# Optimization experiments

Hardware: AMD Instinct MI355X
Metric: run time of the kernel (lower is better)

Reference implementation:

```python
import jax, jax.numpy as jnp
import numpy as np

N, M, E = 50000, 50000, 1600000
D_IN, HID, OUT = 128, 128, 128


def setup_inputs() -> dict:
    key = jax.random.key(0)
    ks = jax.random.split(key, 8)
    query = jax.random.normal(ks[0], (N, D_IN), jnp.float32)
    memory = jax.random.normal(ks[1], (M, D_IN), jnp.float32)
    adj_vals = jnp.ones((E,), jnp.float32)  # tf.sparse adjacency values (typically 1.0)
    Wq = jax.random.normal(ks[2], (D_IN, HID), jnp.float32) * 0.05
    bq = jnp.zeros((HID,), jnp.float32)
    Wk = jax.random.normal(ks[3], (D_IN, HID), jnp.float32) * 0.05
    bk = jnp.zeros((HID,), jnp.float32)
    Wv = jax.random.normal(ks[4], (D_IN, OUT), jnp.float32) * 0.05
    bv = jnp.zeros((OUT,), jnp.float32)
    rows = jnp.sort(jax.random.randint(ks[5], (E,), 0, N, jnp.int32))
    cols = jax.random.randint(ks[6], (E,), 0, M, jnp.int32)
    return {"query": query, "memory": memory, "adj_vals": adj_vals,
            "Wq": Wq, "bq": bq, "Wk": Wk, "bk": bk, "Wv": Wv, "bv": bv,
            "rows": rows, "cols": cols}


def reference(query, memory, adj_vals, Wq, bq, Wk, bk, Wv, bv, rows, cols):
    n = query.shape[0]
    hid = Wq.shape[1]
    # Dense projections with gelu (tfa.activations.gelu default approximate=True)
    q = jax.nn.gelu(query @ Wq + bq, approximate=True)   # [n, hid]
    k = jax.nn.gelu(memory @ Wk + bk, approximate=True)  # [m, hid]
    v = jax.nn.gelu(memory @ Wv + bv, approximate=True)  # [m, out]
    # Edge-level scores = (q_i . k_j) / sqrt(hid) * adj_val  (== coef * adj_matrix)
    scores = jnp.sum(q[rows] * k[cols], axis=-1)          # [E]
    scores = scores * (adj_vals / jnp.sqrt(jnp.float32(hid)))
    # Sparse softmax over nonzero entries of each row (tf.sparse.softmax)
    row_max = jax.ops.segment_max(scores, rows, num_segments=n, indices_are_sorted=True)
    row_max = jnp.where(jnp.isfinite(row_max), row_max, 0.0)  # rows with no edges
    e = jnp.exp(scores - row_max[rows])
    denom = jax.ops.segment_sum(e, rows, num_segments=n, indices_are_sorted=True)
    w = e / denom[rows]                                   # [E]
    # Sparse-dense matmul: out_i = sum_j w_ij * v_j
    out = jax.ops.segment_sum(w[:, None] * v[cols], rows, num_segments=n, indices_are_sorted=True)
    return out
```

## Files before the change

### kernel.cpp

```cpp
#include <hip/hip_runtime.h>
#include <math.h>

typedef _Float16 f16x4 __attribute__((ext_vector_type(4)));
typedef _Float16 f16x8 __attribute__((ext_vector_type(8)));
typedef float f32x4 __attribute__((ext_vector_type(4)));

#define DIM 128
#define LDST 136

#if defined(__has_builtin)
#if __has_builtin(__builtin_amdgcn_sdot4)
#define HAVE_SDOT4 1
#endif
#endif

__device__ __forceinline__ int dot4i8(int a, int b, int c) {
#ifdef HAVE_SDOT4
    return __builtin_amdgcn_sdot4(a, b, c, false);
#else
    int s = c;
#pragma unroll
    for (int j = 0; j < 4; ++j)
        s += (int)((signed char)((a >> (8 * j)) & 0xff)) *
             (int)((signed char)((b >> (8 * j)) & 0xff));
    return s;
#endif
}

__device__ __forceinline__ float i8f(unsigned int w, int j) {
    return (float)((signed char)((w >> (8 * j)) & 0xff));
}

__global__ __launch_bounds__(256) void setup_kernel(
    const float* __restrict__ Wq, const float* __restrict__ Wk,
    const float* __restrict__ Wv, _Float16* __restrict__ Wt,
    const int* __restrict__ rows, int* __restrict__ row_ptr, int n, int e)
{
    int b = blockIdx.x;
    if (b < 192) {
        int mat = b >> 6;
        const float* W = (mat == 0) ? Wq : (mat == 1) ? Wk : Wv;
        _Float16* dst = Wt + (size_t)mat * DIM * DIM;
        int idx = (b & 63) * 256 + threadIdx.x;
        int k = idx >> 7;
        int c = idx & 127;
        dst[c * DIM + k] = (_Float16)W[idx];
    } else {
        int r = (b - 192) * 256 + threadIdx.x;
        if (r > n) return;
        if (r == n) { row_ptr[n] = e; return; }
        int lo = 0, hi = e;
        while (lo < hi) {
            int mid = (lo + hi) >> 1;
            if (rows[mid] < r) lo = mid + 1; else hi = mid;
        }
        row_ptr[r] = lo;
    }
}

__global__ __launch_bounds__(256, 3) void proj_gemm_kernel(
    const float* __restrict__ query, const float* __restrict__ memory,
    const _Float16* __restrict__ Wt,
    const float* __restrict__ bq, const float* __restrict__ bk,
    const float* __restrict__ bv,
    unsigned char* __restrict__ q8i, float* __restrict__ sclq,
    unsigned char* __restrict__ k8i, unsigned char* __restrict__ v8i,
    float2* __restrict__ scl2, int n, int m)
{
    __shared__ _Float16 xs[128 * LDST];

    int which = blockIdx.y;
    const float* X     = (which == 0) ? query : memory;
    const _Float16* Wm = Wt + (size_t)which * DIM * DIM;
    const float* bias  = (which == 0) ? bq : (which == 1) ? bk : bv;
    int R              = (which == 0) ? n : m;

    int tid = threadIdx.x;
    int rowblock = blockIdx.x * 128;
    if (rowblock >= R) return;

    for (int it = 0; it < 16; ++it) {
        int flat = it * 256 + tid;
        int r  = flat >> 5;
        int c4 = (flat & 31) * 4;
        int gr = rowblock + r;
        if (gr >= R) gr = R - 1;
        float4 x = *(const float4*)(X + (size_t)gr * DIM + c4);
        f16x4 w4;
        w4[0] = (_Float16)x.x; w4[1] = (_Float16)x.y;
        w4[2] = (_Float16)x.z; w4[3] = (_Float16)x.w;
        *(f16x4*)(&xs[r * LDST + c4]) = w4;
    }
    __syncthreads();

    int wave = tid >> 6;
    int lane = tid & 63;
    int quad = lane >> 4;
    int l16  = lane & 15;
    int wrow = wave * 32;

    f16x8 afrag[2][4];
    for (int rt = 0; rt < 2; ++rt)
        for (int ks = 0; ks < 4; ++ks)
            afrag[rt][ks] = *(const f16x8*)(&xs[(wrow + rt * 16 + l16) * LDST + quad * 8 + ks * 32]);

    f32x4 acc[8][2];
    for (int ct = 0; ct < 8; ++ct) { acc[ct][0] = {0,0,0,0}; acc[ct][1] = {0,0,0,0}; }
    for (int ct = 0; ct < 8; ++ct) {
        const _Float16* wp = Wm + (size_t)(ct * 16 + l16) * DIM + quad * 8;
        for (int ks = 0; ks < 4; ++ks) {
            f16x8 b = *(const f16x8*)(wp + ks * 32);
            acc[ct][0] = __builtin_amdgcn_mfma_f32_16x16x32_f16(afrag[0][ks], b, acc[ct][0], 0, 0, 0);
            acc[ct][1] = __builtin_amdgcn_mfma_f32_16x16x32_f16(afrag[1][ks], b, acc[ct][1], 0, 0, 0);
        }
    }

    __syncthreads();
    for (int ct = 0; ct < 8; ++ct) {
        float bval = bias[ct * 16 + l16];
        for (int rt = 0; rt < 2; ++rt) {
            for (int reg = 0; reg < 4; ++reg) {
                float x = acc[ct][rt][reg] + bval;
                float t  = 0.7978845608028654f * (x + 0.044715f * x * x * x);
                float th = 1.0f - 2.0f / (__expf(2.0f * t) + 1.0f);
                float g  = 0.5f * x * (1.0f + th);
                xs[(wrow + rt * 16 + quad * 4 + reg) * LDST + ct * 16 + l16] = (_Float16)g;
            }
        }
    }
    __syncthreads();

    unsigned char* Y = (which == 0) ? q8i : (which == 1) ? k8i : v8i;
    for (int it = 0; it < 8; ++it) {
        int flat = it * 256 + tid;
        int r  = flat >> 4;
        int c8 = (flat & 15) * 8;
        int gr = rowblock + r;
        f16x8 h = *(const f16x8*)(&xs[r * LDST + c8]);
        float f[8];
        float mx = 0.0f;
#pragma unroll
        for (int j = 0; j < 8; ++j) {
            f[j] = (float)h[j];
            mx = fmaxf(mx, fabsf(f[j]));
        }
        mx = fmaxf(mx, __shfl_xor(mx, 1));
        mx = fmaxf(mx, __shfl_xor(mx, 2));
        mx = fmaxf(mx, __shfl_xor(mx, 4));
        mx = fmaxf(mx, __shfl_xor(mx, 8));
        float qs = (mx > 0.0f) ? 127.0f / mx : 0.0f;
        if (gr < R) {
            unsigned int w0 = 0, w1 = 0;
#pragma unroll
            for (int j = 0; j < 4; ++j) {
                int q = (int)rintf(fminf(fmaxf(f[j] * qs, -127.0f), 127.0f));
                w0 |= ((unsigned int)(q & 0xff)) << (8 * j);
            }
#pragma unroll
            for (int j = 0; j < 4; ++j) {
                int q = (int)rintf(fminf(fmaxf(f[4 + j] * qs, -127.0f), 127.0f));
                w1 |= ((unsigned int)(q & 0xff)) << (8 * j);
            }
            *(uint2*)(Y + (size_t)gr * DIM + c8) = make_uint2(w0, w1);
            if ((flat & 15) == 0) {
                float ds = mx * (1.0f / 127.0f);
                if (which == 0)      sclq[gr]   = ds;
                else if (which == 1) scl2[gr].x = ds;
                else                 scl2[gr].y = ds;
            }
        }
    }
}

__global__ __launch_bounds__(256) void edge_attn_kernel(
    const unsigned char* __restrict__ q8i, const float* __restrict__ sclq,
    const unsigned char* __restrict__ k8i, const unsigned char* __restrict__ v8i,
    const float2* __restrict__ scl2, const float* __restrict__ adj_vals,
    const int* __restrict__ cols, const int* __restrict__ row_ptr,
    float* __restrict__ out, int n)
{
    int row = blockIdx.x * 4 + (threadIdx.x >> 6);
    if (row >= n) return;
    int lane = threadIdx.x & 63;
    int g    = lane >> 3;
    int d8   = lane & 7;

    int start = row_ptr[row];
    int end   = row_ptr[row + 1];

    int4  qw = *(const int4*)(q8i + (size_t)row * DIM + d8 * 16);
    float sq = sclq[row];

    float s_sum = 0.0f;
    float acc[16];
#pragma unroll
    for (int j = 0; j < 16; ++j) acc[j] = 0.0f;

    const float scale = 0.08838834764831845f;

    for (int gg = start; gg < end; gg += 8) {
        int e     = gg + g;
        bool vld  = e < end;
        int  i    = vld ? e : end - 1;
        int  c    = cols[i];
        float a   = adj_vals[i] * scale;
        float2 sk = scl2[c];

        const unsigned char* base = k8i + (size_t)c * DIM + d8 * 16;
        int4 kw = *(const int4*)base;
        int4 vw = *(const int4*)(v8i + (size_t)c * DIM + d8 * 16);

        int di = dot4i8(qw.x, kw.x, 0);
        di = dot4i8(qw.y, kw.y, di);
        di = dot4i8(qw.z, kw.z, di);
        di = dot4i8(qw.w, kw.w, di);
        di += __shfl_xor(di, 1);
        di += __shfl_xor(di, 2);
        di += __shfl_xor(di, 4);

        float score = (float)di * (sq * sk.x) * a;
        float p = vld ? __expf(score) : 0.0f;
        s_sum += p;

        float psv = p * sk.y;
#pragma unroll
        for (int j = 0; j < 4; ++j) {
            acc[j]      += psv * i8f((unsigned int)vw.x, j);
            acc[4 + j]  += psv * i8f((unsigned int)vw.y, j);
            acc[8 + j]  += psv * i8f((unsigned int)vw.z, j);
            acc[12 + j] += psv * i8f((unsigned int)vw.w, j);
        }
    }

    s_sum += __shfl_xor(s_sum, 8);
    s_sum += __shfl_xor(s_sum, 16);
    s_sum += __shfl_xor(s_sum, 32);
#pragma unroll
    for (int j = 0; j < 16; ++j) {
        acc[j] += __shfl_xor(acc[j], 8);
        acc[j] += __shfl_xor(acc[j], 16);
        acc[j] += __shfl_xor(acc[j], 32);
    }
    float inv = (s_sum > 0.0f) ? 1.0f / s_sum : 0.0f;

    if (g == 0) {
        float4* dst = (float4*)(out + (size_t)row * DIM + d8 * 16);
#pragma unroll
        for (int j = 0; j < 4; ++j)
            dst[j] = make_float4(acc[4 * j] * inv, acc[4 * j + 1] * inv,
                                 acc[4 * j + 2] * inv, acc[4 * j + 3] * inv);
    }
}

extern "C" void kernel_launch(void* const* d_in, const int* in_sizes, int n_in,
                              void* d_out, int out_size, void* d_ws, size_t ws_size,
                              hipStream_t stream)
{
    const float* query    = (const float*)d_in[0];
    const float* memory   = (const float*)d_in[1];
    const float* adj_vals = (const float*)d_in[2];
    const float* Wq       = (const float*)d_in[3];
    const float* bq       = (const float*)d_in[4];
    const float* Wk       = (const float*)d_in[5];
    const float* bk       = (const float*)d_in[6];
    const float* Wv       = (const float*)d_in[7];
    const float* bv       = (const float*)d_in[8];
    const int*   rows     = (const int*)d_in[9];
    const int*   cols     = (const int*)d_in[10];
    float* out = (float*)d_out;

    int n = in_sizes[0] / DIM;
    int m = in_sizes[1] / DIM;
    int e = in_sizes[9];

    char* ws = (char*)d_ws;
    size_t off = 0;
    _Float16* Wt = (_Float16*)(ws + off);       off += (size_t)3 * DIM * DIM * 2;
    unsigned char* q8i = (unsigned char*)(ws + off); off += (size_t)n * DIM;
    unsigned char* k8i = (unsigned char*)(ws + off); off += (size_t)m * DIM;
    unsigned char* v8i = (unsigned char*)(ws + off); off += (size_t)m * DIM;
    float* sclq  = (float*)(ws + off);          off += (size_t)n * 4;
    float2* scl2 = (float2*)(ws + off);         off += (size_t)m * 8;
    int* row_ptr = (int*)(ws + off);            off += (size_t)(n + 1) * 4;

    int rp_blocks = (n + 1 + 255) / 256;
    setup_kernel<<<dim3(192 + rp_blocks), 256, 0, stream>>>(
        Wq, Wk, Wv, Wt, rows, row_ptr, n, e);

    proj_gemm_kernel<<<dim3((n + 127) / 128, 3), 256, 0, stream>>>(
        query, memory, Wt, bq, bk, bv, q8i, sclq, k8i, v8i, scl2, n, m);

    edge_attn_kernel<<<dim3((n + 3) / 4), 256, 0, stream>>>(
        q8i, sclq, k8i, v8i, scl2, adj_vals, cols, row_ptr, out, n);
}
```

Baseline: 221.4 us.

## Interleave K and V rows, use magic-number int8 to fp16 decode and exp2

Stores the quantized K and V for each memory row next to each other in one 256-byte record, so every gathered edge touches one contiguous region instead of two separate arrays. V is stored with a +128 bias so a byte-permute against 0x64 builds fp16 values of 1024+byte directly. The constant offset (1024+128) is removed afterwards using a running sum of the weights. The score scale is folded together with log2(e) so the exponent is a single exp2. These cut the per-edge gather traffic and the per-element integer-to-float conversion cost, at the price of extra bias-correction arithmetic and some fp32 cancellation error from subtracting the large offset.

```diff
diff --git a/kernel.cpp b/kernel.cpp
--- a/kernel.cpp
+++ b/kernel.cpp
@@ -1,18 +1,34 @@
 #include <hip/hip_runtime.h>
 #include <math.h>
 
+typedef _Float16 f16x2 __attribute__((ext_vector_type(2)));
 typedef _Float16 f16x4 __attribute__((ext_vector_type(4)));
 typedef _Float16 f16x8 __attribute__((ext_vector_type(8)));
 typedef float f32x4 __attribute__((ext_vector_type(4)));
 
 #define DIM 128
 #define LDST 136
+#define KVR 256
 
 #if defined(__has_builtin)
 #if __has_builtin(__builtin_amdgcn_sdot4)
 #define HAVE_SDOT4 1
 #endif
-#endif
+#if __has_builtin(__builtin_amdgcn_perm)
+#define HAVE_PERM 1
+#endif
+#if __has_builtin(__builtin_amdgcn_exp2f)
+#define HAVE_EXP2 1
+#endif
+#endif
+
+__device__ __forceinline__ float fast_exp2(float x) {
+#ifdef HAVE_EXP2
+    return __builtin_amdgcn_exp2f(x);
+#else
+    return exp2f(x);
+#endif
+}
 
 __device__ __forceinline__ int dot4i8(int a, int b, int c) {
 #ifdef HAVE_SDOT4
@@ -27,8 +43,18 @@
 #endif
 }
 
-__device__ __forceinline__ float i8f(unsigned int w, int j) {
-    return (float)((signed char)((w >> (8 * j)) & 0xff));
+union U32H2 { unsigned int u; f16x2 h; };
+
+__device__ __forceinline__ f16x2 byte2f16(unsigned int w, unsigned int sel) {
+    U32H2 u;
+#ifdef HAVE_PERM
+    u.u = __builtin_amdgcn_perm(0x64646464u, w, sel);
+#else
+    unsigned b0 = (w >> (8 * (sel & 3))) & 0xff;
+    unsigned b1 = (w >> (8 * ((sel >> 16) & 3))) & 0xff;
+    u.u = 0x64006400u | b0 | (b1 << 16);
+#endif
+    return u.h;
 }
 
 __global__ __launch_bounds__(256) void setup_kernel(
@@ -64,8 +90,8 @@
     const float* __restrict__ bq, const float* __restrict__ bk,
     const float* __restrict__ bv,
     unsigned char* __restrict__ q8i, float* __restrict__ sclq,
-    unsigned char* __restrict__ k8i, unsigned char* __restrict__ v8i,
-    float2* __restrict__ scl2, int n, int m)
+    unsigned char* __restrict__ kv, float2* __restrict__ scl2,
+    int n, int m)
 {
     __shared__ _Float16 xs[128 * LDST];
 
@@ -130,7 +156,7 @@
     }
     __syncthreads();
 
-    unsigned char* Y = (which == 0) ? q8i : (which == 1) ? k8i : v8i;
+    int qbias = (which == 2) ? 128 : 0;
     for (int it = 0; it < 8; ++it) {
         int flat = it * 256 + tid;
         int r  = flat >> 4;
@@ -153,15 +179,20 @@
             unsigned int w0 = 0, w1 = 0;
 #pragma unroll
             for (int j = 0; j < 4; ++j) {
-                int q = (int)rintf(fminf(fmaxf(f[j] * qs, -127.0f), 127.0f));
+                int q = (int)rintf(fminf(fmaxf(f[j] * qs, -127.0f), 127.0f)) + qbias;
                 w0 |= ((unsigned int)(q & 0xff)) << (8 * j);
             }
 #pragma unroll
             for (int j = 0; j < 4; ++j) {
-                int q = (int)rintf(fminf(fmaxf(f[4 + j] * qs, -127.0f), 127.0f));
+                int q = (int)rintf(fminf(fmaxf(f[4 + j] * qs, -127.0f), 127.0f)) + qbias;
                 w1 |= ((unsigned int)(q & 0xff)) << (8 * j);
             }
-            *(uint2*)(Y + (size_t)gr * DIM + c8) = make_uint2(w0, w1);
+            if (which == 0)
+                *(uint2*)(q8i + (size_t)gr * DIM + c8) = make_uint2(w0, w1);
+            else if (which == 1)
+                *(uint2*)(kv + (size_t)gr * KVR + c8) = make_uint2(w0, w1);
+            else
+                *(uint2*)(kv + (size_t)gr * KVR + 128 + c8) = make_uint2(w0, w1);
             if ((flat & 15) == 0) {
                 float ds = mx * (1.0f / 127.0f);
                 if (which == 0)      sclq[gr]   = ds;
@@ -174,10 +205,9 @@
 
 __global__ __launch_bounds__(256) void edge_attn_kernel(
     const unsigned char* __restrict__ q8i, const float* __restrict__ sclq,
-    const unsigned char* __restrict__ k8i, const unsigned char* __restrict__ v8i,
-    const float2* __restrict__ scl2, const float* __restrict__ adj_vals,
-    const int* __restrict__ cols, const int* __restrict__ row_ptr,
-    float* __restrict__ out, int n)
+    const unsigned char* __restrict__ kv, const float2* __restrict__ scl2,
+    const float* __restrict__ adj_vals, const int* __restrict__ cols,
+    const int* __restrict__ row_ptr, float* __restrict__ out, int n)
 {
     int row = blockIdx.x * 4 + (threadIdx.x >> 6);
     if (row >= n) return;
@@ -189,26 +219,25 @@
     int end   = row_ptr[row + 1];
 
     int4  qw = *(const int4*)(q8i + (size_t)row * DIM + d8 * 16);
-    float sq = sclq[row];
+    float csr = sclq[row] * (0.08838834764831845f * 1.442695040888963f);
 
     float s_sum = 0.0f;
+    float spsv  = 0.0f;
     float acc[16];
 #pragma unroll
     for (int j = 0; j < 16; ++j) acc[j] = 0.0f;
-
-    const float scale = 0.08838834764831845f;
 
     for (int gg = start; gg < end; gg += 8) {
         int e     = gg + g;
         bool vld  = e < end;
         int  i    = vld ? e : end - 1;
         int  c    = cols[i];
-        float a   = adj_vals[i] * scale;
+        float a   = adj_vals[i];
         float2 sk = scl2[c];
 
-        const unsigned char* base = k8i + (size_t)c * DIM + d8 * 16;
+        const unsigned char* base = kv + (size_t)c * KVR + d8 * 16;
         int4 kw = *(const int4*)base;
-        int4 vw = *(const int4*)(v8i + (size_t)c * DIM + d8 * 16);
+        int4 vw = *(const int4*)(base + 128);
 
         int di = dot4i8(qw.x, kw.x, 0);
         di = dot4i8(qw.y, kw.y, di);
@@ -218,19 +247,26 @@
         di += __shfl_xor(di, 2);
         di += __shfl_xor(di, 4);
 
-        float score = (float)di * (sq * sk.x) * a;
-        float p = vld ? __expf(score) : 0.0f;
+        float p = vld ? fast_exp2((float)di * (csr * sk.x * a)) : 0.0f;
         s_sum += p;
 
         float psv = p * sk.y;
-#pragma unroll
-        for (int j = 0; j < 4; ++j) {
-            acc[j]      += psv * i8f((unsigned int)vw.x, j);
-            acc[4 + j]  += psv * i8f((unsigned int)vw.y, j);
-            acc[8 + j]  += psv * i8f((unsigned int)vw.z, j);
-            acc[12 + j] += psv * i8f((unsigned int)vw.w, j);
-        }
-    }
+        spsv += psv;
+#pragma unroll
+        for (int d = 0; d < 4; ++d) {
+            unsigned int w = (d == 0) ? (unsigned int)vw.x : (d == 1) ? (unsigned int)vw.y
+                           : (d == 2) ? (unsigned int)vw.z : (unsigned int)vw.w;
+            f16x2 lo = byte2f16(w, 0x04010400u);
+            f16x2 hi = byte2f16(w, 0x04030402u);
+            acc[4 * d]     += psv * (float)lo[0];
+            acc[4 * d + 1] += psv * (float)lo[1];
+            acc[4 * d + 2] += psv * (float)hi[0];
+            acc[4 * d + 3] += psv * (float)hi[1];
+        }
+    }
+
+#pragma unroll
+    for (int j = 0; j < 16; ++j) acc[j] -= 1152.0f * spsv;
 
     s_sum += __shfl_xor(s_sum, 8);
     s_sum += __shfl_xor(s_sum, 16);
@@ -275,21 +311,20 @@
 
     char* ws = (char*)d_ws;
     size_t off = 0;
-    _Float16* Wt = (_Float16*)(ws + off);       off += (size_t)3 * DIM * DIM * 2;
+    _Float16* Wt = (_Float16*)(ws + off);            off += (size_t)3 * DIM * DIM * 2;
     unsigned char* q8i = (unsigned char*)(ws + off); off += (size_t)n * DIM;
-    unsigned char* k8i = (unsigned char*)(ws + off); off += (size_t)m * DIM;
-    unsigned char* v8i = (unsigned char*)(ws + off); off += (size_t)m * DIM;
-    float* sclq  = (float*)(ws + off);          off += (size_t)n * 4;
-    float2* scl2 = (float2*)(ws + off);         off += (size_t)m * 8;
-    int* row_ptr = (int*)(ws + off);            off += (size_t)(n + 1) * 4;
+    unsigned char* kv  = (unsigned char*)(ws + off); off += (size_t)m * KVR;
+    float* sclq  = (float*)(ws + off);               off += (size_t)n * 4;
+    float2* scl2 = (float2*)(ws + off);              off += (size_t)m * 8;
+    int* row_ptr = (int*)(ws + off);                 off += (size_t)(n + 1) * 4;
 
     int rp_blocks = (n + 1 + 255) / 256;
     setup_kernel<<<dim3(192 + rp_blocks), 256, 0, stream>>>(
         Wq, Wk, Wv, Wt, rows, row_ptr, n, e);
 
     proj_gemm_kernel<<<dim3((n + 127) / 128, 3), 256, 0, stream>>>(
-        query, memory, Wt, bq, bk, bv, q8i, sclq, k8i, v8i, scl2, n, m);
+        query, memory, Wt, bq, bk, bv, q8i, sclq, kv, scl2, n, m);
 
     edge_attn_kernel<<<dim3((n + 3) / 4), 256, 0, stream>>>(
-        q8i, sclq, k8i, v8i, scl2, adj_vals, cols, row_ptr, out, n);
-}
+        q8i, sclq, kv, scl2, adj_vals, cols, row_ptr, out, n);
+}
```

Result: no change. 218.8 us, median of 2 (-1.2%).
